# Performance work log

Measured on AMD Instinct MI355X. Metric: run time of the kernel, lower is better.

Reference implementation:

```python
import jax, jax.numpy as jnp
import numpy as np

A, U, ANT, D2, H = 128, 8, 64, 64, 256
NUE = A * U            # 1024 ues
E_INT = A * NUE        # 131072 interferes edges (all ap x ue pairs)
E_DL = NUE             # one d_link edge per ue


def _mlp(x, Wa, ba, Wb, bb):
    return jax.nn.relu(x @ Wa + ba) @ Wb + bb


def setup_inputs() -> dict:
    key = jax.random.key(0)
    ks = jax.random.split(key, 14)
    f32 = jnp.float32
    inp = {
        'pl_int_re': jax.random.normal(ks[0], (E_INT, ANT), f32) * 0.1,
        'pl_int_im': jax.random.normal(ks[1], (E_INT, ANT), f32) * 0.1,
        'pl_dl_re': jax.random.normal(ks[2], (E_DL, ANT), f32) * 0.1,
        'pl_dl_im': jax.random.normal(ks[3], (E_DL, ANT), f32) * 0.1,
        'pv_re': jax.random.normal(ks[4], (A, U, ANT), f32) * 0.1,
        'pv_im': jax.random.normal(ks[5], (A, U, ANT), f32) * 0.1,
        'W2a': jax.random.normal(ks[6], (4 * ANT, H), f32) / np.sqrt(4 * ANT),
        'b2a': jnp.zeros((H,), f32),
        'W2b': jax.random.normal(ks[7], (H, D2), f32) / np.sqrt(H),
        'b2b': jnp.zeros((D2,), f32),
        'W1a': jax.random.normal(ks[8], (1 + 2 * ANT + D2, H), f32) / np.sqrt(1 + 2 * ANT + D2),
        'b1a': jnp.zeros((H,), f32),
        'W1b': jax.random.normal(ks[9], (H, 2 * ANT), f32) / np.sqrt(H),
        'b1b': jnp.zeros((2 * ANT,), f32),
        # interferes: every ap -> every ue
        'int_src': jnp.repeat(jnp.arange(A, dtype=jnp.int32), NUE),
        'int_dst': jnp.tile(jnp.arange(NUE, dtype=jnp.int32), A),
        # d_link: ap a -> ues [a*U, (a+1)*U)
        'dl_src': jnp.repeat(jnp.arange(A, dtype=jnp.int32), U),
        'dl_dst': jnp.arange(NUE, dtype=jnp.int32),
    }
    return inp


def reference(pl_int_re, pl_int_im, pl_dl_re, pl_dl_im, pv_re, pv_im,
              W2a, b2a, W2b, b2b, W1a, b1a, W1b, b1b,
              int_src, int_dst, dl_src, dl_dst):
    pv = jax.lax.complex(pv_re, pv_im)            # [A,U,ANT] ap power_vector
    pl_int = jax.lax.complex(pl_int_re, pl_int_im)  # [E_INT,ANT]
    pl_dl = jax.lax.complex(pl_dl_re, pl_dl_im)     # [E_DL,ANT]

    def aggregate_interferes(pv_cur):
        src_sum = jnp.sum(pv_cur, axis=1)[int_src]              # [E,ANT]
        infer_vec = src_sum.conj() * pl_int                      # [E,ANT]
        sum_ap = jnp.sum(jnp.abs(infer_vec) ** 2, axis=-1)       # ||.||^2 -> [E]
        return jax.ops.segment_sum(sum_ap[:, None], int_dst, num_segments=NUE)  # [NUE,1]

    # 1) aggregate_interferes (stored in graph; recomputed at the end)
    _ = aggregate_interferes(pv)

    # 2) mlp_aggregate_interferes
    src_sum = jnp.sum(pv, axis=1)[int_src]                       # [E,ANT] complex
    feats = jnp.concatenate([pl_int, src_sum], axis=1)           # [E,2*ANT] complex
    cat_feats = jnp.concatenate([feats.real, feats.imag], axis=1)  # [E,4*ANT]
    msg2 = _mlp(cat_feats, W2a, b2a, W2b, b2b)                   # [E,D2]
    mlp_ue_all = jax.ops.segment_sum(msg2, int_dst, num_segments=NUE)  # [NUE,D2]

    # 3) update_ue_power_vector (d_link edges)
    src_pv_dl = pv[dl_src]                                       # [E_DL,U,ANT]
    iner = jnp.einsum('eua,ea->eu', src_pv_dl.conj(), pl_dl)     # bmm -> [E_DL,U]
    norm1 = jnp.abs(iner) ** 2                                   # [E_DL,U]
    mask1 = jnp.ones((E_DL, U), norm1.dtype).at[jnp.arange(E_DL), dl_dst % U].set(0.0)
    in_infer = jnp.sum(norm1 * mask1, axis=1)[:, None]           # [E_DL,1]

    feat1 = jnp.concatenate([in_infer, pl_dl.real, pl_dl.imag, mlp_ue_all[dl_dst]], axis=1)
    out1 = _mlp(feat1, W1a, b1a, W1b, b1b).reshape(E_DL, 2, ANT)  # [E_DL,2,ANT]
    ue_pv_msg = jax.lax.complex(out1[:, 0, :], out1[:, 1, :])    # [E_DL,ANT]
    # each ue receives exactly one message
    ue_pv = jnp.zeros((NUE, ANT), ue_pv_msg.dtype).at[dl_dst].set(ue_pv_msg)

    # 4) update_ap_power_vector (u_link: ue i -> ap i//U; mailbox [A,U,ANT])
    mailbox = ue_pv.reshape(A, U, ANT)
    flat = mailbox.reshape(A, U * ANT)
    row_sums = jnp.sum(jnp.abs(flat), axis=-1, keepdims=True)
    pv_new = (flat / row_sums).reshape(A, U, ANT)

    # 5) final aggregate_interferes with updated power vectors
    ue_all_interference = aggregate_interferes(pv_new)

    out_stacked = jnp.stack([pv_new.real, pv_new.imag])          # [2,A,U,ANT]
    return out_stacked, ue_all_interference
```

## Files before the change

### kernel.cpp

```cpp
#include <hip/hip_runtime.h>
#include <hip/hip_bf16.h>
#include <hip/hip_fp16.h>

#define A_NUM 128
#define U_NUM 8
#define ANT 64
#define D2 64
#define H_DIM 256
#define NUE 1024
#define E_INT 131072

typedef __attribute__((ext_vector_type(8))) short bf16x8_t;
typedef __attribute__((ext_vector_type(4))) float f32x4_t;

static __device__ inline unsigned short f2bf(float x) {
    unsigned int u = __float_as_uint(x);
    unsigned int r = (u + 0x7fffu + ((u >> 16) & 1u)) >> 16;
    return (unsigned short)r;
}
static __device__ inline unsigned int pack2(float a, float b) {
    return (unsigned int)f2bf(a) | ((unsigned int)f2bf(b) << 16);
}
static __device__ inline float bf2f(unsigned short s) {
    return __uint_as_float(((unsigned int)s) << 16);
}

__global__ void prep_kernel(const float* __restrict__ pv_re, const float* __restrict__ pv_im,
                            const float* __restrict__ W2a, const float* __restrict__ b2a,
                            const float* __restrict__ W2b,
                            const float* __restrict__ W1a, const float* __restrict__ W1b,
                            float* __restrict__ Sa, unsigned short* __restrict__ WpT,
                            unsigned short* __restrict__ W2bT,
                            float* __restrict__ W1aT, float* __restrict__ W1bT) {
    int bid = blockIdx.x, t = threadIdx.x;
    if (bid < A_NUM) {
        __shared__ float sre[ANT], sim[ANT];
        if (t < ANT) {
            float s = 0.f;
            for (int u = 0; u < U_NUM; ++u) s += pv_re[bid * 512 + u * 64 + t];
            sre[t] = s;
        } else if (t < 2 * ANT) {
            int ant = t - ANT;
            float s = 0.f;
            for (int u = 0; u < U_NUM; ++u) s += pv_im[bid * 512 + u * 64 + ant];
            sim[ant] = s;
        }
        __syncthreads();
        float a0 = 0.f, a1 = 0.f, a2 = 0.f, a3 = 0.f;
        for (int ant = 0; ant < ANT; ant += 2) {
            a0 += sre[ant] * W2a[(64 + ant) * H_DIM + t];
            a1 += sim[ant] * W2a[(192 + ant) * H_DIM + t];
            a2 += sre[ant + 1] * W2a[(64 + ant + 1) * H_DIM + t];
            a3 += sim[ant + 1] * W2a[(192 + ant + 1) * H_DIM + t];
        }
        Sa[bid * H_DIM + t] = b2a[t] + ((a0 + a2) + (a1 + a3));
    } else if (bid < 136) {
        int base = (bid - A_NUM) * 256 + t;
        for (int i = base; i < 32768 + 16384; i += 8 * 256) {
            if (i < 32768) {
                int h = i >> 7, k = i & 127;
                int row = (k < 64) ? k : (k + 64);
                WpT[i] = f2bf(W2a[row * H_DIM + h]);
            } else {
                int i2 = i - 32768;
                int d = i2 >> 8, k2 = i2 & 255;
                W2bT[i2] = f2bf(W2b[k2 * D2 + d]);
            }
        }
    } else {
        for (int i = (bid - 136) * 256 + t; i < 53248 + 32768; i += 32 * 256) {
            if (i < 53248) {
                int k = i >> 8, h = i & 255;
                W1aT[h * 208 + k] = (k < 193) ? W1a[k * 256 + h] : 0.f;
            } else {
                int i2 = i - 53248;
                int k = i2 >> 7, c = i2 & 127;
                W1bT[c * 256 + k] = W1b[k * 128 + c];
            }
        }
    }
}

__global__ __launch_bounds__(256, 4) void mlp2_kernel(
        const float* __restrict__ plre, const float* __restrict__ plim,
        const float* __restrict__ Sa, const unsigned short* __restrict__ WpT,
        const unsigned short* __restrict__ W2bT, float* __restrict__ partial,
        unsigned short* __restrict__ Pws) {
    __shared__ __attribute__((aligned(16))) unsigned short F2[2][16 * 136];
    __shared__ __attribute__((aligned(16))) unsigned short Hl[16][264];
    int bid = blockIdx.x;
    int ac = bid >> 6, jt = bid & 63;
    int j0 = jt * 16, a0 = ac * 8;
    int t = threadIdx.x, w = t >> 6, l = t & 63, lm = l & 15, lk = l >> 4;

    bf16x8_t bfr[4][4];
#pragma unroll
    for (int ht = 0; ht < 4; ++ht)
#pragma unroll
        for (int kc = 0; kc < 4; ++kc)
            bfr[ht][kc] = *reinterpret_cast<const bf16x8_t*>(
                WpT + (w * 64 + ht * 16 + lm) * 128 + kc * 32 + lk * 8);
    bf16x8_t b2h[8];
#pragma unroll
    for (int kcl = 0; kcl < 8; ++kcl)
        b2h[kcl] = *reinterpret_cast<const bf16x8_t*>(
            W2bT + (w * 16 + lm) * 256 + kcl * 32 + lk * 8);

    int er = t >> 4, seg = t & 15;
    const float* stage_base = (seg < 8) ? plre : plim;
    int stage_off = (j0 + er) * 64 + (seg & 7) * 8;
    int fw = er * 136 + seg * 8;

    f32x4_t acc2 = (f32x4_t){0.f, 0.f, 0.f, 0.f};

    float4 s0, s1;
    {
        const float* p = stage_base + (size_t)a0 * 65536 + stage_off;
        s0 = *reinterpret_cast<const float4*>(p);
        s1 = *reinterpret_cast<const float4*>(p + 4);
        *reinterpret_cast<uint4*>(&F2[0][fw]) =
            make_uint4(pack2(s0.x, s0.y), pack2(s0.z, s0.w),
                       pack2(s1.x, s1.y), pack2(s1.z, s1.w));
    }
    {
        const float* p = stage_base + (size_t)(a0 + 1) * 65536 + stage_off;
        s0 = *reinterpret_cast<const float4*>(p);
        s1 = *reinterpret_cast<const float4*>(p + 4);
    }

    int cur = 0;
    for (int ai = 0; ai < 8; ++ai) {
        int a = a0 + ai;
        __syncthreads();
        const unsigned short* Fc = F2[cur];
        if (t < 128) {
            int er3 = t >> 3, seg3 = t & 7;
            uint4 rr = *reinterpret_cast<const uint4*>(Fc + er3 * 136 + seg3 * 8);
            uint4 ri = *reinterpret_cast<const uint4*>(Fc + er3 * 136 + 64 + seg3 * 8);
            const unsigned short* pr = (const unsigned short*)&rr;
            const unsigned short* pi = (const unsigned short*)&ri;
            unsigned int pk[4];
#pragma unroll
            for (int i = 0; i < 4; ++i) {
                float re0 = bf2f(pr[2 * i]), im0 = bf2f(pi[2 * i]);
                float re1 = bf2f(pr[2 * i + 1]), im1 = bf2f(pi[2 * i + 1]);
                unsigned short h0 = __half_as_ushort(__float2half(re0 * re0 + im0 * im0));
                unsigned short h1 = __half_as_ushort(__float2half(re1 * re1 + im1 * im1));
                pk[i] = (unsigned int)h0 | ((unsigned int)h1 << 16);
            }
            *reinterpret_cast<uint4*>(&Pws[(unsigned)(a * 1024 + j0 + er3) * 64 + seg3 * 8]) =
                make_uint4(pk[0], pk[1], pk[2], pk[3]);
        }
        f32x4_t acc1[4];
#pragma unroll
        for (int ht = 0; ht < 4; ++ht) {
            float sa = Sa[a * H_DIM + w * 64 + ht * 16 + lm];
            acc1[ht] = (f32x4_t){sa, sa, sa, sa};
        }
#pragma unroll
        for (int kc = 0; kc < 4; ++kc) {
            bf16x8_t afr = *reinterpret_cast<const bf16x8_t*>(Fc + lm * 136 + kc * 32 + lk * 8);
#pragma unroll
            for (int ht = 0; ht < 4; ++ht)
                acc1[ht] = __builtin_amdgcn_mfma_f32_16x16x32_bf16(afr, bfr[ht][kc], acc1[ht], 0, 0, 0);
        }
#pragma unroll
        for (int ht = 0; ht < 4; ++ht)
#pragma unroll
            for (int r = 0; r < 4; ++r) {
                float v = acc1[ht][r];
                Hl[lk * 4 + r][ht * 16 + lm + w * 64] = f2bf(v > 0.f ? v : 0.f);
            }
        __syncthreads();
#pragma unroll
        for (int kcl = 0; kcl < 8; ++kcl) {
            bf16x8_t a2 = *reinterpret_cast<const bf16x8_t*>(&Hl[lm][kcl * 32 + lk * 8]);
            acc2 = __builtin_amdgcn_mfma_f32_16x16x32_bf16(a2, b2h[kcl], acc2, 0, 0, 0);
        }
        if (ai < 7) {
            *reinterpret_cast<uint4*>(&F2[cur ^ 1][fw]) =
                make_uint4(pack2(s0.x, s0.y), pack2(s0.z, s0.w),
                           pack2(s1.x, s1.y), pack2(s1.z, s1.w));
            if (ai < 6) {
                const float* p = stage_base + (size_t)(a0 + ai + 2) * 65536 + stage_off;
                s0 = *reinterpret_cast<const float4*>(p);
                s1 = *reinterpret_cast<const float4*>(p + 4);
            }
            cur ^= 1;
        }
    }
#pragma unroll
    for (int r = 0; r < 4; ++r)
        partial[ac * 65536 + (j0 + lk * 4 + r) * 64 + w * 16 + lm] = acc2[r];
}

__global__ __launch_bounds__(512) void dlink_norm(
        const float* __restrict__ pv_re, const float* __restrict__ pv_im,
        const float* __restrict__ pldre, const float* __restrict__ pldim,
        const float* __restrict__ partial, const float* __restrict__ b2b,
        const float* __restrict__ W1aT, const float* __restrict__ b1a,
        const float* __restrict__ W1bT, const float* __restrict__ b1b,
        float* __restrict__ Q, float* __restrict__ out) {
    int a = blockIdx.x, t = threadIdx.x, w = t >> 6, l = t & 63;
    __shared__ float pvr[512], pvi[512], pldr[512], pldi[512];
    __shared__ float nrm[8][8];
    __shared__ __attribute__((aligned(16))) float feat[8][212];
    __shared__ __attribute__((aligned(16))) float h1[8][260];
    __shared__ float red2[2][8][128];
    __shared__ __attribute__((aligned(16))) float o1[8][128];
    __shared__ float redn[8];
    __shared__ float SshInv;

    pvr[t] = pv_re[a * 512 + t];
    pvi[t] = pv_im[a * 512 + t];
    pldr[t] = pldre[a * 512 + t];
    pldi[t] = pldim[a * 512 + t];
    {
        float acc = 128.f * b2b[t & 63];
#pragma unroll
        for (int c = 0; c < 16; ++c) acc += partial[c * 65536 + a * 512 + t];
        feat[t >> 6][129 + (t & 63)] = acc;
    }
    if (t < 152) feat[t / 19][193 + t % 19] = 0.f;
    __syncthreads();
    feat[t >> 6][1 + (t & 63)] = pldr[t];
    feat[t >> 6][65 + (t & 63)] = pldi[t];
#pragma unroll
    for (int p = 0; p < 8; ++p) {
        int idx = w * 8 + p;
        int el = idx >> 3, u = idx & 7;
        float pr = pvr[u * 64 + l], pi = pvi[u * 64 + l];
        float qr = pldr[el * 64 + l], qi = pldi[el * 64 + l];
        float ir = pr * qr + pi * qi;
        float ii = pr * qi - pi * qr;
        for (int m = 1; m < 64; m <<= 1) {
            ir += __shfl_xor(ir, m, 64);
            ii += __shfl_xor(ii, m, 64);
        }
        if (l == 0) nrm[el][u] = ir * ir + ii * ii;
    }
    __syncthreads();
    if (t < 8) {
        float s = 0.f;
        for (int u = 0; u < 8; ++u)
            if (u != t) s += nrm[t][u];
        feat[t][0] = s;
    }
    __syncthreads();
    {
        int h = t >> 1, e0 = (t & 1) * 4;
        const float4* wrow = reinterpret_cast<const float4*>(W1aT + h * 208);
        const float4* f0p = reinterpret_cast<const float4*>(&feat[e0 + 0][0]);
        const float4* f1p = reinterpret_cast<const float4*>(&feat[e0 + 1][0]);
        const float4* f2p = reinterpret_cast<const float4*>(&feat[e0 + 2][0]);
        const float4* f3p = reinterpret_cast<const float4*>(&feat[e0 + 3][0]);
        float ac0 = 0.f, ac1 = 0.f, ac2 = 0.f, ac3 = 0.f;
#pragma unroll 4
        for (int kq = 0; kq < 52; ++kq) {
            float4 wv = wrow[kq];
            float4 f0 = f0p[kq], f1 = f1p[kq], f2 = f2p[kq], f3 = f3p[kq];
            ac0 = fmaf(wv.x, f0.x, ac0); ac0 = fmaf(wv.y, f0.y, ac0);
            ac0 = fmaf(wv.z, f0.z, ac0); ac0 = fmaf(wv.w, f0.w, ac0);
            ac1 = fmaf(wv.x, f1.x, ac1); ac1 = fmaf(wv.y, f1.y, ac1);
            ac1 = fmaf(wv.z, f1.z, ac1); ac1 = fmaf(wv.w, f1.w, ac1);
            ac2 = fmaf(wv.x, f2.x, ac2); ac2 = fmaf(wv.y, f2.y, ac2);
            ac2 = fmaf(wv.z, f2.z, ac2); ac2 = fmaf(wv.w, f2.w, ac2);
            ac3 = fmaf(wv.x, f3.x, ac3); ac3 = fmaf(wv.y, f3.y, ac3);
            ac3 = fmaf(wv.z, f3.z, ac3); ac3 = fmaf(wv.w, f3.w, ac3);
        }
        float bb = b1a[h];
        float s0 = bb + ac0, s1 = bb + ac1, s2 = bb + ac2, s3 = bb + ac3;
        h1[e0 + 0][h] = s0 > 0.f ? s0 : 0.f;
        h1[e0 + 1][h] = s1 > 0.f ? s1 : 0.f;
        h1[e0 + 2][h] = s2 > 0.f ? s2 : 0.f;
        h1[e0 + 3][h] = s3 > 0.f ? s3 : 0.f;
    }
    __syncthreads();
    {
        int e0 = (t & 1) * 4, c = (t >> 1) & 127, kh = t >> 8;
        const float4* wrow = reinterpret_cast<const float4*>(W1bT + c * 256 + kh * 128);
        const float4* g0 = reinterpret_cast<const float4*>(&h1[e0 + 0][kh * 128]);
        const float4* g1 = reinterpret_cast<const float4*>(&h1[e0 + 1][kh * 128]);
        const float4* g2 = reinterpret_cast<const float4*>(&h1[e0 + 2][kh * 128]);
        const float4* g3 = reinterpret_cast<const float4*>(&h1[e0 + 3][kh * 128]);
        float ac0 = 0.f, ac1 = 0.f, ac2 = 0.f, ac3 = 0.f;
#pragma unroll 4
        for (int kq = 0; kq < 32; ++kq) {
            float4 wv = wrow[kq];
            float4 f0 = g0[kq], f1 = g1[kq], f2 = g2[kq], f3 = g3[kq];
            ac0 = fmaf(wv.x, f0.x, ac0); ac0 = fmaf(wv.y, f0.y, ac0);
            ac0 = fmaf(wv.z, f0.z, ac0); ac0 = fmaf(wv.w, f0.w, ac0);
            ac1 = fmaf(wv.x, f1.x, ac1); ac1 = fmaf(wv.y, f1.y, ac1);
            ac1 = fmaf(wv.z, f1.z, ac1); ac1 = fmaf(wv.w, f1.w, ac1);
            ac2 = fmaf(wv.x, f2.x, ac2); ac2 = fmaf(wv.y, f2.y, ac2);
            ac2 = fmaf(wv.z, f2.z, ac2); ac2 = fmaf(wv.w, f2.w, ac2);
            ac3 = fmaf(wv.x, f3.x, ac3); ac3 = fmaf(wv.y, f3.y, ac3);
            ac3 = fmaf(wv.z, f3.z, ac3); ac3 = fmaf(wv.w, f3.w, ac3);
        }
        red2[kh][e0 + 0][c] = ac0;
        red2[kh][e0 + 1][c] = ac1;
        red2[kh][e0 + 2][c] = ac2;
        red2[kh][e0 + 3][c] = ac3;
    }
    __syncthreads();
    {
        int i0 = t, i1 = t + 512;
        o1[i0 >> 7][i0 & 127] = b1b[i0 & 127] + red2[0][i0 >> 7][i0 & 127] + red2[1][i0 >> 7][i0 & 127];
        o1[i1 >> 7][i1 & 127] = b1b[i1 & 127] + red2[0][i1 >> 7][i1 & 127] + red2[1][i1 >> 7][i1 & 127];
    }
    __syncthreads();
    {
        int el = t >> 6, ant = t & 63;
        float re = o1[el][ant], im = o1[el][64 + ant];
        float v = sqrtf(re * re + im * im);
        for (int m = 1; m < 64; m <<= 1) v += __shfl_xor(v, m, 64);
        if (l == 0) redn[w] = v;
    }
    __syncthreads();
    if (t == 0) {
        float S = redn[0] + redn[1] + redn[2] + redn[3] +
                  redn[4] + redn[5] + redn[6] + redn[7];
        SshInv = 1.f / S;
    }
    __syncthreads();
    {
        float inv = SshInv;
        int el = t >> 6, ant = t & 63;
        out[a * 512 + t] = o1[el][ant] * inv;
        out[65536 + a * 512 + t] = o1[el][64 + ant] * inv;
        if (t < 64) {
            float sr = 0.f, si = 0.f;
#pragma unroll
            for (int u = 0; u < 8; ++u) {
                sr += o1[u][t];
                si += o1[u][64 + t];
            }
            sr *= inv;
            si *= inv;
            Q[a * 64 + t] = sr * sr + si * si;
        }
    }
}

__global__ __launch_bounds__(256) void final_agg(const unsigned short* __restrict__ Pws,
                                                 const float* __restrict__ Qv,
                                                 float* __restrict__ out) {
    int bid = blockIdx.x, t = threadIdx.x, w = t >> 6, l = t & 63;
    __shared__ __attribute__((aligned(16))) float Qc[128][68];
    for (int i = t; i < 8192; i += 256) Qc[i >> 6][i & 63] = Qv[i];
    __syncthreads();
    int j = bid * 4 + w;
    int as = l >> 3, og = l & 7;
    float acc = 0.f;
#pragma unroll 4
    for (int ab = 0; ab < 16; ++ab) {
        int aa = ab * 8 + as;
        uint4 pv4 = *reinterpret_cast<const uint4*>(&Pws[(unsigned)(aa * 1024 + j) * 64 + og * 8]);
        float4 q0 = *reinterpret_cast<const float4*>(&Qc[aa][og * 8]);
        float4 q1 = *reinterpret_cast<const float4*>(&Qc[aa][og * 8 + 4]);
        const unsigned short* hp = (const unsigned short*)&pv4;
        acc += __half2float(__ushort_as_half(hp[0])) * q0.x;
        acc += __half2float(__ushort_as_half(hp[1])) * q0.y;
        acc += __half2float(__ushort_as_half(hp[2])) * q0.z;
        acc += __half2float(__ushort_as_half(hp[3])) * q0.w;
        acc += __half2float(__ushort_as_half(hp[4])) * q1.x;
        acc += __half2float(__ushort_as_half(hp[5])) * q1.y;
        acc += __half2float(__ushort_as_half(hp[6])) * q1.z;
        acc += __half2float(__ushort_as_half(hp[7])) * q1.w;
    }
    for (int m = 1; m < 64; m <<= 1) acc += __shfl_xor(acc, m, 64);
    if (l == 0) out[131072 + j] = acc;
}

extern "C" void kernel_launch(void* const* d_in, const int* in_sizes, int n_in,
                              void* d_out, int out_size, void* d_ws, size_t ws_size,
                              hipStream_t stream) {
    const float* plre = (const float*)d_in[0];
    const float* plim = (const float*)d_in[1];
    const float* pldre = (const float*)d_in[2];
    const float* pldim = (const float*)d_in[3];
    const float* pvre = (const float*)d_in[4];
    const float* pvim = (const float*)d_in[5];
    const float* W2a = (const float*)d_in[6];
    const float* b2a = (const float*)d_in[7];
    const float* W2b = (const float*)d_in[8];
    const float* b2b = (const float*)d_in[9];
    const float* W1a = (const float*)d_in[10];
    const float* b1a = (const float*)d_in[11];
    const float* W1b = (const float*)d_in[12];
    const float* b1b = (const float*)d_in[13];

    char* ws = (char*)d_ws;
    float* Sa = (float*)(ws);
    unsigned short* WpT = (unsigned short*)(ws + 131072);
    unsigned short* W2bT = (unsigned short*)(ws + 196608);
    float* Q = (float*)(ws + 229376);
    float* partial = (float*)(ws + 262144);
    unsigned short* Pws = (unsigned short*)(ws + 4456448);
    float* W1aT = (float*)(ws + 21233664);
    float* W1bT = (float*)(ws + 21446656);
    float* out = (float*)d_out;

    prep_kernel<<<168, 256, 0, stream>>>(pvre, pvim, W2a, b2a, W2b, W1a, W1b,
                                         Sa, WpT, W2bT, W1aT, W1bT);
    mlp2_kernel<<<1024, 256, 0, stream>>>(plre, plim, Sa, WpT, W2bT, partial, Pws);
    dlink_norm<<<128, 512, 0, stream>>>(pvre, pvim, pldre, pldim, partial, b2b,
                                        W1aT, b1a, W1bT, b1b, Q, out);
    final_agg<<<256, 256, 0, stream>>>(Pws, Q, out);
}
```

Measured before the change: 78.70 us.

## Split hidden dim across 8 waves, load A-fragments directly, reduce partials via LDS

```diff
diff --git a/kernel.cpp b/kernel.cpp
--- a/kernel.cpp
+++ b/kernel.cpp
@@ -21,8 +21,17 @@
 static __device__ inline unsigned int pack2(float a, float b) {
     return (unsigned int)f2bf(a) | ((unsigned int)f2bf(b) << 16);
 }
-static __device__ inline float bf2f(unsigned short s) {
-    return __uint_as_float(((unsigned int)s) << 16);
+static __device__ inline bf16x8_t pack8(float4 a, float4 b) {
+    union { unsigned int u[4]; bf16x8_t v; } r;
+    r.u[0] = pack2(a.x, a.y);
+    r.u[1] = pack2(a.z, a.w);
+    r.u[2] = pack2(b.x, b.y);
+    r.u[3] = pack2(b.z, b.w);
+    return r.v;
+}
+static __device__ inline unsigned int packh2(float a, float b) {
+    return (unsigned int)__half_as_ushort(__float2half(a)) |
+           ((unsigned int)__half_as_ushort(__float2half(b)) << 16);
 }
 
 __global__ void prep_kernel(const float* __restrict__ pv_re, const float* __restrict__ pv_im,
@@ -81,117 +90,110 @@
     }
 }
 
-__global__ __launch_bounds__(256, 4) void mlp2_kernel(
+__global__ __launch_bounds__(512, 4) void mlp2_kernel(
         const float* __restrict__ plre, const float* __restrict__ plim,
         const float* __restrict__ Sa, const unsigned short* __restrict__ WpT,
         const unsigned short* __restrict__ W2bT, float* __restrict__ partial,
         unsigned short* __restrict__ Pws) {
-    __shared__ __attribute__((aligned(16))) unsigned short F2[2][16 * 136];
-    __shared__ __attribute__((aligned(16))) unsigned short Hl[16][264];
+    __shared__ __attribute__((aligned(16))) float smraw[8 * 16 * 68];
     int bid = blockIdx.x;
     int ac = bid >> 6, jt = bid & 63;
     int j0 = jt * 16, a0 = ac * 8;
     int t = threadIdx.x, w = t >> 6, l = t & 63, lm = l & 15, lk = l >> 4;
-
-    bf16x8_t bfr[4][4];
-#pragma unroll
-    for (int ht = 0; ht < 4; ++ht)
+    int h0 = w * 32;
+
+    bf16x8_t bfr[2][4];
+#pragma unroll
+    for (int ht = 0; ht < 2; ++ht)
 #pragma unroll
         for (int kc = 0; kc < 4; ++kc)
             bfr[ht][kc] = *reinterpret_cast<const bf16x8_t*>(
-                WpT + (w * 64 + ht * 16 + lm) * 128 + kc * 32 + lk * 8);
-    bf16x8_t b2h[8];
-#pragma unroll
-    for (int kcl = 0; kcl < 8; ++kcl)
-        b2h[kcl] = *reinterpret_cast<const bf16x8_t*>(
-            W2bT + (w * 16 + lm) * 256 + kcl * 32 + lk * 8);
-
-    int er = t >> 4, seg = t & 15;
-    const float* stage_base = (seg < 8) ? plre : plim;
-    int stage_off = (j0 + er) * 64 + (seg & 7) * 8;
-    int fw = er * 136 + seg * 8;
-
-    f32x4_t acc2 = (f32x4_t){0.f, 0.f, 0.f, 0.f};
-
-    float4 s0, s1;
-    {
-        const float* p = stage_base + (size_t)a0 * 65536 + stage_off;
-        s0 = *reinterpret_cast<const float4*>(p);
-        s1 = *reinterpret_cast<const float4*>(p + 4);
-        *reinterpret_cast<uint4*>(&F2[0][fw]) =
-            make_uint4(pack2(s0.x, s0.y), pack2(s0.z, s0.w),
-                       pack2(s1.x, s1.y), pack2(s1.z, s1.w));
-    }
-    {
-        const float* p = stage_base + (size_t)(a0 + 1) * 65536 + stage_off;
-        s0 = *reinterpret_cast<const float4*>(p);
-        s1 = *reinterpret_cast<const float4*>(p + 4);
-    }
-
-    int cur = 0;
+                WpT + (h0 + ht * 16 + lm) * 128 + kc * 32 + lk * 8);
+    bf16x8_t b2h[4];
+#pragma unroll
+    for (int dt = 0; dt < 4; ++dt)
+        b2h[dt] = *reinterpret_cast<const bf16x8_t*>(
+            W2bT + (dt * 16 + lm) * 256 + h0 + lk * 8);
+
+    unsigned short* Hw = reinterpret_cast<unsigned short*>(smraw) + w * (16 * 40);
+    f32x4_t acc2[4];
+#pragma unroll
+    for (int dt = 0; dt < 4; ++dt) acc2[dt] = (f32x4_t){0.f, 0.f, 0.f, 0.f};
+
     for (int ai = 0; ai < 8; ++ai) {
         int a = a0 + ai;
-        __syncthreads();
-        const unsigned short* Fc = F2[cur];
-        if (t < 128) {
-            int er3 = t >> 3, seg3 = t & 7;
-            uint4 rr = *reinterpret_cast<const uint4*>(Fc + er3 * 136 + seg3 * 8);
-            uint4 ri = *reinterpret_cast<const uint4*>(Fc + er3 * 136 + 64 + seg3 * 8);
-            const unsigned short* pr = (const unsigned short*)&rr;
-            const unsigned short* pi = (const unsigned short*)&ri;
-            unsigned int pk[4];
-#pragma unroll
-            for (int i = 0; i < 4; ++i) {
-                float re0 = bf2f(pr[2 * i]), im0 = bf2f(pi[2 * i]);
-                float re1 = bf2f(pr[2 * i + 1]), im1 = bf2f(pi[2 * i + 1]);
-                unsigned short h0 = __half_as_ushort(__float2half(re0 * re0 + im0 * im0));
-                unsigned short h1 = __half_as_ushort(__float2half(re1 * re1 + im1 * im1));
-                pk[i] = (unsigned int)h0 | ((unsigned int)h1 << 16);
-            }
-            *reinterpret_cast<uint4*>(&Pws[(unsigned)(a * 1024 + j0 + er3) * 64 + seg3 * 8]) =
-                make_uint4(pk[0], pk[1], pk[2], pk[3]);
-        }
-        f32x4_t acc1[4];
-#pragma unroll
-        for (int ht = 0; ht < 4; ++ht) {
-            float sa = Sa[a * H_DIM + w * 64 + ht * 16 + lm];
-            acc1[ht] = (f32x4_t){sa, sa, sa, sa};
-        }
-#pragma unroll
-        for (int kc = 0; kc < 4; ++kc) {
-            bf16x8_t afr = *reinterpret_cast<const bf16x8_t*>(Fc + lm * 136 + kc * 32 + lk * 8);
-#pragma unroll
-            for (int ht = 0; ht < 4; ++ht)
-                acc1[ht] = __builtin_amdgcn_mfma_f32_16x16x32_bf16(afr, bfr[ht][kc], acc1[ht], 0, 0, 0);
-        }
-#pragma unroll
-        for (int ht = 0; ht < 4; ++ht)
-#pragma unroll
-            for (int r = 0; r < 4; ++r) {
-                float v = acc1[ht][r];
-                Hl[lk * 4 + r][ht * 16 + lm + w * 64] = f2bf(v > 0.f ? v : 0.f);
-            }
-        __syncthreads();
-#pragma unroll
-        for (int kcl = 0; kcl < 8; ++kcl) {
-            bf16x8_t a2 = *reinterpret_cast<const bf16x8_t*>(&Hl[lm][kcl * 32 + lk * 8]);
-            acc2 = __builtin_amdgcn_mfma_f32_16x16x32_bf16(a2, b2h[kcl], acc2, 0, 0, 0);
-        }
-        if (ai < 7) {
-            *reinterpret_cast<uint4*>(&F2[cur ^ 1][fw]) =
-                make_uint4(pack2(s0.x, s0.y), pack2(s0.z, s0.w),
-                           pack2(s1.x, s1.y), pack2(s1.z, s1.w));
-            if (ai < 6) {
-                const float* p = stage_base + (size_t)(a0 + ai + 2) * 65536 + stage_off;
-                s0 = *reinterpret_cast<const float4*>(p);
-                s1 = *reinterpret_cast<const float4*>(p + 4);
-            }
-            cur ^= 1;
-        }
-    }
-#pragma unroll
-    for (int r = 0; r < 4; ++r)
-        partial[ac * 65536 + (j0 + lk * 4 + r) * 64 + w * 16 + lm] = acc2[r];
+        const float* rowre = plre + (size_t)(a * 1024 + j0 + lm) * 64;
+        const float* rowim = plim + (size_t)(a * 1024 + j0 + lm) * 64;
+        float4 r0 = *reinterpret_cast<const float4*>(rowre + lk * 8);
+        float4 r1 = *reinterpret_cast<const float4*>(rowre + lk * 8 + 4);
+        float4 r2 = *reinterpret_cast<const float4*>(rowre + 32 + lk * 8);
+        float4 r3 = *reinterpret_cast<const float4*>(rowre + 32 + lk * 8 + 4);
+        float4 i0 = *reinterpret_cast<const float4*>(rowim + lk * 8);
+        float4 i1 = *reinterpret_cast<const float4*>(rowim + lk * 8 + 4);
+        float4 i2 = *reinterpret_cast<const float4*>(rowim + 32 + lk * 8);
+        float4 i3 = *reinterpret_cast<const float4*>(rowim + 32 + lk * 8 + 4);
+
+        if (w == 0) {
+            unsigned short* pd = Pws + (unsigned)(a * 1024 + j0 + lm) * 64 + lk * 8;
+            *reinterpret_cast<uint4*>(pd) = make_uint4(
+                packh2(r0.x * r0.x + i0.x * i0.x, r0.y * r0.y + i0.y * i0.y),
+                packh2(r0.z * r0.z + i0.z * i0.z, r0.w * r0.w + i0.w * i0.w),
+                packh2(r1.x * r1.x + i1.x * i1.x, r1.y * r1.y + i1.y * i1.y),
+                packh2(r1.z * r1.z + i1.z * i1.z, r1.w * r1.w + i1.w * i1.w));
+            *reinterpret_cast<uint4*>(pd + 32) = make_uint4(
+                packh2(r2.x * r2.x + i2.x * i2.x, r2.y * r2.y + i2.y * i2.y),
+                packh2(r2.z * r2.z + i2.z * i2.z, r2.w * r2.w + i2.w * i2.w),
+                packh2(r3.x * r3.x + i3.x * i3.x, r3.y * r3.y + i3.y * i3.y),
+                packh2(r3.z * r3.z + i3.z * i3.z, r3.w * r3.w + i3.w * i3.w));
+        }
+
+        bf16x8_t fa0 = pack8(r0, r1);
+        bf16x8_t fa1 = pack8(r2, r3);
+        bf16x8_t fa2 = pack8(i0, i1);
+        bf16x8_t fa3 = pack8(i2, i3);
+
+        float sa0 = Sa[a * H_DIM + h0 + lm];
+        float sa1 = Sa[a * H_DIM + h0 + 16 + lm];
+        f32x4_t acc1a = (f32x4_t){sa0, sa0, sa0, sa0};
+        f32x4_t acc1b = (f32x4_t){sa1, sa1, sa1, sa1};
+        acc1a = __builtin_amdgcn_mfma_f32_16x16x32_bf16(fa0, bfr[0][0], acc1a, 0, 0, 0);
+        acc1b = __builtin_amdgcn_mfma_f32_16x16x32_bf16(fa0, bfr[1][0], acc1b, 0, 0, 0);
+        acc1a = __builtin_amdgcn_mfma_f32_16x16x32_bf16(fa1, bfr[0][1], acc1a, 0, 0, 0);
+        acc1b = __builtin_amdgcn_mfma_f32_16x16x32_bf16(fa1, bfr[1][1], acc1b, 0, 0, 0);
+        acc1a = __builtin_amdgcn_mfma_f32_16x16x32_bf16(fa2, bfr[0][2], acc1a, 0, 0, 0);
+        acc1b = __builtin_amdgcn_mfma_f32_16x16x32_bf16(fa2, bfr[1][2], acc1b, 0, 0, 0);
+        acc1a = __builtin_amdgcn_mfma_f32_16x16x32_bf16(fa3, bfr[0][3], acc1a, 0, 0, 0);
+        acc1b = __builtin_amdgcn_mfma_f32_16x16x32_bf16(fa3, bfr[1][3], acc1b, 0, 0, 0);
+
+#pragma unroll
+        for (int r = 0; r < 4; ++r) {
+            int j = lk * 4 + r;
+            float va = acc1a[r], vb = acc1b[r];
+            Hw[j * 40 + lm] = f2bf(va > 0.f ? va : 0.f);
+            Hw[j * 40 + 16 + lm] = f2bf(vb > 0.f ? vb : 0.f);
+        }
+        bf16x8_t a2 = *reinterpret_cast<const bf16x8_t*>(Hw + lm * 40 + lk * 8);
+#pragma unroll
+        for (int dt = 0; dt < 4; ++dt)
+            acc2[dt] = __builtin_amdgcn_mfma_f32_16x16x32_bf16(a2, b2h[dt], acc2[dt], 0, 0, 0);
+    }
+
+    __syncthreads();
+    float* red = smraw;
+#pragma unroll
+    for (int dt = 0; dt < 4; ++dt)
+#pragma unroll
+        for (int r = 0; r < 4; ++r)
+            red[(w * 16 + lk * 4 + r) * 68 + dt * 16 + lm] = acc2[dt][r];
+    __syncthreads();
+    for (int i = t; i < 1024; i += 512) {
+        int j = i >> 6, d = i & 63;
+        float s0 = red[(0 * 16 + j) * 68 + d] + red[(1 * 16 + j) * 68 + d];
+        float s1 = red[(2 * 16 + j) * 68 + d] + red[(3 * 16 + j) * 68 + d];
+        float s2 = red[(4 * 16 + j) * 68 + d] + red[(5 * 16 + j) * 68 + d];
+        float s3 = red[(6 * 16 + j) * 68 + d] + red[(7 * 16 + j) * 68 + d];
+        partial[ac * 65536 + (j0 + j) * 64 + d] = (s0 + s1) + (s2 + s3);
+    }
 }
 
 __global__ __launch_bounds__(512) void dlink_norm(
@@ -266,7 +268,7 @@
             ac2 = fmaf(wv.x, f2.x, ac2); ac2 = fmaf(wv.y, f2.y, ac2);
             ac2 = fmaf(wv.z, f2.z, ac2); ac2 = fmaf(wv.w, f2.w, ac2);
             ac3 = fmaf(wv.x, f3.x, ac3); ac3 = fmaf(wv.y, f3.y, ac3);
-            ac3 = fmaf(wv.z, f3.z, ac3); ac3 = fmaf(wv.w, f3.w, ac3);
+            ac3 = fmaf(wv.w, f3.w, ac3); ac3 = fmaf(wv.z, f3.z, ac3);
         }
         float bb = b1a[h];
         float s0 = bb + ac0, s1 = bb + ac1, s2 = bb + ac2, s3 = bb + ac3;
@@ -403,7 +405,7 @@
 
     prep_kernel<<<168, 256, 0, stream>>>(pvre, pvim, W2a, b2a, W2b, W1a, W1b,
                                          Sa, WpT, W2bT, W1aT, W1bT);
-    mlp2_kernel<<<1024, 256, 0, stream>>>(plre, plim, Sa, WpT, W2bT, partial, Pws);
+    mlp2_kernel<<<1024, 512, 0, stream>>>(plre, plim, Sa, WpT, W2bT, partial, Pws);
     dlink_norm<<<128, 512, 0, stream>>>(pvre, pvim, pldre, pldim, partial, b2b,
                                         W1aT, b1a, W1bT, b1b, Q, out);
     final_agg<<<256, 256, 0, stream>>>(Pws, Q, out);
```

Result: slower. 111.2 us (+41.3%).

## Retile mlp2 kernel: split hidden dim across blocks, stage MFMA-fragment weights in LDS

Applied to the files above, without the earlier changes.

```diff
diff --git a/kernel.cpp b/kernel.cpp
--- a/kernel.cpp
+++ b/kernel.cpp
@@ -21,16 +21,17 @@
 static __device__ inline unsigned int pack2(float a, float b) {
     return (unsigned int)f2bf(a) | ((unsigned int)f2bf(b) << 16);
 }
-static __device__ inline float bf2f(unsigned short s) {
-    return __uint_as_float(((unsigned int)s) << 16);
+static __device__ inline unsigned int packh2(float a, float b) {
+    return (unsigned int)__half_as_ushort(__float2half(a)) |
+           ((unsigned int)__half_as_ushort(__float2half(b)) << 16);
 }
 
 __global__ void prep_kernel(const float* __restrict__ pv_re, const float* __restrict__ pv_im,
                             const float* __restrict__ W2a, const float* __restrict__ b2a,
                             const float* __restrict__ W2b,
                             const float* __restrict__ W1a, const float* __restrict__ W1b,
-                            float* __restrict__ Sa, unsigned short* __restrict__ WpT,
-                            unsigned short* __restrict__ W2bT,
+                            float* __restrict__ Sa, unsigned short* __restrict__ WpF,
+                            unsigned short* __restrict__ W2bF,
                             float* __restrict__ W1aT, float* __restrict__ W1bT) {
     int bid = blockIdx.x, t = threadIdx.x;
     if (bid < A_NUM) {
@@ -56,15 +57,21 @@
         Sa[bid * H_DIM + t] = b2a[t] + ((a0 + a2) + (a1 + a3));
     } else if (bid < 136) {
         int base = (bid - A_NUM) * 256 + t;
-        for (int i = base; i < 32768 + 16384; i += 8 * 256) {
-            if (i < 32768) {
-                int h = i >> 7, k = i & 127;
+        for (int f = base; f < 32768 + 16384; f += 8 * 256) {
+            if (f < 32768) {
+                int i = f & 7, lml = (f >> 3) & 15, lkl = (f >> 7) & 3;
+                int kc = (f >> 9) & 3, ht = (f >> 11) & 1, w = (f >> 12) & 3, hh = (f >> 14) & 1;
+                int h = hh * 128 + w * 32 + ht * 16 + lml;
+                int k = kc * 32 + lkl * 8 + i;
                 int row = (k < 64) ? k : (k + 64);
-                WpT[i] = f2bf(W2a[row * H_DIM + h]);
+                WpF[f] = f2bf(W2a[row * H_DIM + h]);
             } else {
-                int i2 = i - 32768;
-                int d = i2 >> 8, k2 = i2 & 255;
-                W2bT[i2] = f2bf(W2b[k2 * D2 + d]);
+                int f2 = f - 32768;
+                int i = f2 & 7, lml = (f2 >> 3) & 15, lkl = (f2 >> 7) & 3;
+                int dt = (f2 >> 9) & 3, w = (f2 >> 11) & 3, hh = (f2 >> 13) & 1;
+                int d = dt * 16 + lml;
+                int k = hh * 128 + w * 32 + lkl * 8 + i;
+                W2bF[f2] = f2bf(W2b[k * D2 + d]);
             }
         }
     } else {
@@ -81,117 +88,161 @@
     }
 }
 
-__global__ __launch_bounds__(256, 4) void mlp2_kernel(
+__global__ __launch_bounds__(256) void mlp2_kernel(
         const float* __restrict__ plre, const float* __restrict__ plim,
-        const float* __restrict__ Sa, const unsigned short* __restrict__ WpT,
-        const unsigned short* __restrict__ W2bT, float* __restrict__ partial,
+        const float* __restrict__ Sa, const unsigned short* __restrict__ WpF,
+        const unsigned short* __restrict__ W2bF, float* __restrict__ partial,
         unsigned short* __restrict__ Pws) {
-    __shared__ __attribute__((aligned(16))) unsigned short F2[2][16 * 136];
-    __shared__ __attribute__((aligned(16))) unsigned short Hl[16][264];
+    __shared__ __attribute__((aligned(16))) unsigned short Wl[16384];
+    __shared__ __attribute__((aligned(16))) unsigned short W2l[8192];
+    __shared__ __attribute__((aligned(16))) unsigned short F2[2][4352];
+    __shared__ __attribute__((aligned(16))) unsigned short Hw_all[4][1280];
     int bid = blockIdx.x;
-    int ac = bid >> 6, jt = bid & 63;
-    int j0 = jt * 16, a0 = ac * 8;
+    int ac = bid >> 6, hh = (bid >> 5) & 1, jt = bid & 31;
+    int j0 = jt * 32, a0 = ac * 8;
     int t = threadIdx.x, w = t >> 6, l = t & 63, lm = l & 15, lk = l >> 4;
 
-    bf16x8_t bfr[4][4];
-#pragma unroll
-    for (int ht = 0; ht < 4; ++ht)
-#pragma unroll
-        for (int kc = 0; kc < 4; ++kc)
-            bfr[ht][kc] = *reinterpret_cast<const bf16x8_t*>(
-                WpT + (w * 64 + ht * 16 + lm) * 128 + kc * 32 + lk * 8);
-    bf16x8_t b2h[8];
-#pragma unroll
-    for (int kcl = 0; kcl < 8; ++kcl)
-        b2h[kcl] = *reinterpret_cast<const bf16x8_t*>(
-            W2bT + (w * 16 + lm) * 256 + kcl * 32 + lk * 8);
-
-    int er = t >> 4, seg = t & 15;
-    const float* stage_base = (seg < 8) ? plre : plim;
-    int stage_off = (j0 + er) * 64 + (seg & 7) * 8;
-    int fw = er * 136 + seg * 8;
-
-    f32x4_t acc2 = (f32x4_t){0.f, 0.f, 0.f, 0.f};
-
-    float4 s0, s1;
-    {
-        const float* p = stage_base + (size_t)a0 * 65536 + stage_off;
+    {
+        const uint4* srcW = reinterpret_cast<const uint4*>(WpF + hh * 16384);
+        const uint4* srcW2 = reinterpret_cast<const uint4*>(W2bF + hh * 8192);
+        uint4* dW = reinterpret_cast<uint4*>(Wl);
+        uint4* dW2 = reinterpret_cast<uint4*>(W2l);
+        for (int q = t; q < 3072; q += 256) {
+            if (q < 2048) dW[q] = srcW[q];
+            else dW2[q - 2048] = srcW2[q - 2048];
+        }
+    }
+
+    int er = t >> 3, sg = t & 7;
+    const float* sb = (sg < 4) ? plre : plim;
+    int soff = (j0 + er) * 64 + (sg & 3) * 16;
+    int fw = er * 136 + sg * 16;
+
+    unsigned short* Hw = Hw_all[w];
+    f32x4_t acc2[4][2];
+#pragma unroll
+    for (int dt = 0; dt < 4; ++dt)
+#pragma unroll
+        for (int jg = 0; jg < 2; ++jg) acc2[dt][jg] = (f32x4_t){0.f, 0.f, 0.f, 0.f};
+
+    float4 s0, s1, s2, s3;
+    {
+        const float* p = sb + (size_t)a0 * 65536 + soff;
         s0 = *reinterpret_cast<const float4*>(p);
         s1 = *reinterpret_cast<const float4*>(p + 4);
+        s2 = *reinterpret_cast<const float4*>(p + 8);
+        s3 = *reinterpret_cast<const float4*>(p + 12);
         *reinterpret_cast<uint4*>(&F2[0][fw]) =
             make_uint4(pack2(s0.x, s0.y), pack2(s0.z, s0.w),
                        pack2(s1.x, s1.y), pack2(s1.z, s1.w));
-    }
-    {
-        const float* p = stage_base + (size_t)(a0 + 1) * 65536 + stage_off;
+        *reinterpret_cast<uint4*>(&F2[0][fw + 8]) =
+            make_uint4(pack2(s2.x, s2.y), pack2(s2.z, s2.w),
+                       pack2(s3.x, s3.y), pack2(s3.z, s3.w));
+    }
+    {
+        const float* p = sb + (size_t)(a0 + 1) * 65536 + soff;
         s0 = *reinterpret_cast<const float4*>(p);
         s1 = *reinterpret_cast<const float4*>(p + 4);
-    }
+        s2 = *reinterpret_cast<const float4*>(p + 8);
+        s3 = *reinterpret_cast<const float4*>(p + 12);
+    }
+    __syncthreads();
 
     int cur = 0;
     for (int ai = 0; ai < 8; ++ai) {
         int a = a0 + ai;
-        __syncthreads();
         const unsigned short* Fc = F2[cur];
-        if (t < 128) {
-            int er3 = t >> 3, seg3 = t & 7;
-            uint4 rr = *reinterpret_cast<const uint4*>(Fc + er3 * 136 + seg3 * 8);
-            uint4 ri = *reinterpret_cast<const uint4*>(Fc + er3 * 136 + 64 + seg3 * 8);
+
+        if (hh == 0) {
+            uint4 rr = *reinterpret_cast<const uint4*>(Fc + er * 136 + sg * 8);
+            uint4 ri = *reinterpret_cast<const uint4*>(Fc + er * 136 + 64 + sg * 8);
             const unsigned short* pr = (const unsigned short*)&rr;
             const unsigned short* pi = (const unsigned short*)&ri;
             unsigned int pk[4];
 #pragma unroll
             for (int i = 0; i < 4; ++i) {
-                float re0 = bf2f(pr[2 * i]), im0 = bf2f(pi[2 * i]);
-                float re1 = bf2f(pr[2 * i + 1]), im1 = bf2f(pi[2 * i + 1]);
-                unsigned short h0 = __half_as_ushort(__float2half(re0 * re0 + im0 * im0));
-                unsigned short h1 = __half_as_ushort(__float2half(re1 * re1 + im1 * im1));
-                pk[i] = (unsigned int)h0 | ((unsigned int)h1 << 16);
-            }
-            *reinterpret_cast<uint4*>(&Pws[(unsigned)(a * 1024 + j0 + er3) * 64 + seg3 * 8]) =
+                float re0 = __uint_as_float(((unsigned int)pr[2 * i]) << 16);
+                float im0 = __uint_as_float(((unsigned int)pi[2 * i]) << 16);
+                float re1 = __uint_as_float(((unsigned int)pr[2 * i + 1]) << 16);
+                float im1 = __uint_as_float(((unsigned int)pi[2 * i + 1]) << 16);
+                pk[i] = packh2(re0 * re0 + im0 * im0, re1 * re1 + im1 * im1);
+            }
+            *reinterpret_cast<uint4*>(&Pws[(unsigned)(a * 1024 + j0 + er) * 64 + sg * 8]) =
                 make_uint4(pk[0], pk[1], pk[2], pk[3]);
         }
-        f32x4_t acc1[4];
-#pragma unroll
-        for (int ht = 0; ht < 4; ++ht) {
-            float sa = Sa[a * H_DIM + w * 64 + ht * 16 + lm];
-            acc1[ht] = (f32x4_t){sa, sa, sa, sa};
-        }
+
+        float sa0 = Sa[a * H_DIM + hh * 128 + w * 32 + lm];
+        float sa1 = Sa[a * H_DIM + hh * 128 + w * 32 + 16 + lm];
+        f32x4_t acc1[2][2];
+        acc1[0][0] = (f32x4_t){sa0, sa0, sa0, sa0};
+        acc1[1][0] = acc1[0][0];
+        acc1[0][1] = (f32x4_t){sa1, sa1, sa1, sa1};
+        acc1[1][1] = acc1[0][1];
 #pragma unroll
         for (int kc = 0; kc < 4; ++kc) {
-            bf16x8_t afr = *reinterpret_cast<const bf16x8_t*>(Fc + lm * 136 + kc * 32 + lk * 8);
-#pragma unroll
-            for (int ht = 0; ht < 4; ++ht)
-                acc1[ht] = __builtin_amdgcn_mfma_f32_16x16x32_bf16(afr, bfr[ht][kc], acc1[ht], 0, 0, 0);
-        }
-#pragma unroll
-        for (int ht = 0; ht < 4; ++ht)
-#pragma unroll
-            for (int r = 0; r < 4; ++r) {
-                float v = acc1[ht][r];
-                Hl[lk * 4 + r][ht * 16 + lm + w * 64] = f2bf(v > 0.f ? v : 0.f);
-            }
-        __syncthreads();
-#pragma unroll
-        for (int kcl = 0; kcl < 8; ++kcl) {
-            bf16x8_t a2 = *reinterpret_cast<const bf16x8_t*>(&Hl[lm][kcl * 32 + lk * 8]);
-            acc2 = __builtin_amdgcn_mfma_f32_16x16x32_bf16(a2, b2h[kcl], acc2, 0, 0, 0);
+            bf16x8_t b0 = *reinterpret_cast<const bf16x8_t*>(Wl + ((w * 2 + 0) * 4 + kc) * 512 + l * 8);
+            bf16x8_t b1 = *reinterpret_cast<const bf16x8_t*>(Wl + ((w * 2 + 1) * 4 + kc) * 512 + l * 8);
+            bf16x8_t aA = *reinterpret_cast<const bf16x8_t*>(Fc + lm * 136 + kc * 32 + lk * 8);
+            bf16x8_t aB = *reinterpret_cast<const bf16x8_t*>(Fc + (16 + lm) * 136 + kc * 32 + lk * 8);
+            acc1[0][0] = __builtin_amdgcn_mfma_f32_16x16x32_bf16(aA, b0, acc1[0][0], 0, 0, 0);
+            acc1[0][1] = __builtin_amdgcn_mfma_f32_16x16x32_bf16(aA, b1, acc1[0][1], 0, 0, 0);
+            acc1[1][0] = __builtin_amdgcn_mfma_f32_16x16x32_bf16(aB, b0, acc1[1][0], 0, 0, 0);
+            acc1[1][1] = __builtin_amdgcn_mfma_f32_16x16x32_bf16(aB, b1, acc1[1][1], 0, 0, 0);
+        }
+#pragma unroll
+        for (int jg = 0; jg < 2; ++jg)
+#pragma unroll
+            for (int ht = 0; ht < 2; ++ht)
+#pragma unroll
+                for (int r = 0; r < 4; ++r) {
+                    float v = acc1[jg][ht][r];
+                    Hw[(jg * 16 + lk * 4 + r) * 40 + ht * 16 + lm] = f2bf(v > 0.f ? v : 0.f);
+                }
+        {
+            bf16x8_t a20 = *reinterpret_cast<const bf16x8_t*>(Hw + lm * 40 + lk * 8);
+            bf16x8_t a21 = *reinterpret_cast<const bf16x8_t*>(Hw + (16 + lm) * 40 + lk * 8);
+#pragma unroll
+            for (int dt = 0; dt < 4; ++dt) {
+                bf16x8_t b2 = *reinterpret_cast<const bf16x8_t*>(W2l + (w * 4 + dt) * 512 + l * 8);
+                acc2[dt][0] = __builtin_amdgcn_mfma_f32_16x16x32_bf16(a20, b2, acc2[dt][0], 0, 0, 0);
+                acc2[dt][1] = __builtin_amdgcn_mfma_f32_16x16x32_bf16(a21, b2, acc2[dt][1], 0, 0, 0);
+            }
         }
         if (ai < 7) {
             *reinterpret_cast<uint4*>(&F2[cur ^ 1][fw]) =
                 make_uint4(pack2(s0.x, s0.y), pack2(s0.z, s0.w),
                            pack2(s1.x, s1.y), pack2(s1.z, s1.w));
+            *reinterpret_cast<uint4*>(&F2[cur ^ 1][fw + 8]) =
+                make_uint4(pack2(s2.x, s2.y), pack2(s2.z, s2.w),
+                           pack2(s3.x, s3.y), pack2(s3.z, s3.w));
             if (ai < 6) {
-                const float* p = stage_base + (size_t)(a0 + ai + 2) * 65536 + stage_off;
+                const float* p = sb + (size_t)(a0 + ai + 2) * 65536 + soff;
                 s0 = *reinterpret_cast<const float4*>(p);
                 s1 = *reinterpret_cast<const float4*>(p + 4);
-            }
+                s2 = *reinterpret_cast<const float4*>(p + 8);
+                s3 = *reinterpret_cast<const float4*>(p + 12);
+            }
+            __syncthreads();
             cur ^= 1;
         }
     }
-#pragma unroll
-    for (int r = 0; r < 4; ++r)
-        partial[ac * 65536 + (j0 + lk * 4 + r) * 64 + w * 16 + lm] = acc2[r];
+
+    __syncthreads();
+    float* red = reinterpret_cast<float*>(Wl);
+#pragma unroll
+    for (int dt = 0; dt < 4; ++dt)
+#pragma unroll
+        for (int jg = 0; jg < 2; ++jg)
+#pragma unroll
+            for (int r = 0; r < 4; ++r)
+                red[(w * 32 + jg * 16 + lk * 4 + r) * 64 + dt * 16 + lm] = acc2[dt][jg][r];
+    __syncthreads();
+    for (int idx = t; idx < 2048; idx += 256) {
+        int j = idx >> 6, d = idx & 63;
+        float s = (red[(0 * 32 + j) * 64 + d] + red[(1 * 32 + j) * 64 + d]) +
+                  (red[(2 * 32 + j) * 64 + d] + red[(3 * 32 + j) * 64 + d]);
+        partial[(hh * 16 + ac) * 65536 + (j0 + j) * 64 + d] = s;
+    }
 }
 
 __global__ __launch_bounds__(512) void dlink_norm(
@@ -218,7 +269,7 @@
     {
         float acc = 128.f * b2b[t & 63];
 #pragma unroll
-        for (int c = 0; c < 16; ++c) acc += partial[c * 65536 + a * 512 + t];
+        for (int c = 0; c < 32; ++c) acc += partial[c * 65536 + a * 512 + t];
         feat[t >> 6][129 + (t & 63)] = acc;
     }
     if (t < 152) feat[t / 19][193 + t % 19] = 0.f;
@@ -392,18 +443,18 @@
 
     char* ws = (char*)d_ws;
     float* Sa = (float*)(ws);
-    unsigned short* WpT = (unsigned short*)(ws + 131072);
-    unsigned short* W2bT = (unsigned short*)(ws + 196608);
+    unsigned short* WpF = (unsigned short*)(ws + 131072);
+    unsigned short* W2bF = (unsigned short*)(ws + 196608);
     float* Q = (float*)(ws + 229376);
-    float* partial = (float*)(ws + 262144);
-    unsigned short* Pws = (unsigned short*)(ws + 4456448);
-    float* W1aT = (float*)(ws + 21233664);
-    float* W1bT = (float*)(ws + 21446656);
+    float* W1aT = (float*)(ws + 262144);
+    float* W1bT = (float*)(ws + 475136);
+    float* partial = (float*)(ws + 606208);
+    unsigned short* Pws = (unsigned short*)(ws + 8994816);
     float* out = (float*)d_out;
 
     prep_kernel<<<168, 256, 0, stream>>>(pvre, pvim, W2a, b2a, W2b, W1a, W1b,
-                                         Sa, WpT, W2bT, W1aT, W1bT);
-    mlp2_kernel<<<1024, 256, 0, stream>>>(plre, plim, Sa, WpT, W2bT, partial, Pws);
+                                         Sa, WpF, W2bF, W1aT, W1bT);
+    mlp2_kernel<<<1024, 256, 0, stream>>>(plre, plim, Sa, WpF, W2bF, partial, Pws);
     dlink_norm<<<128, 512, 0, stream>>>(pvre, pvim, pldre, pldim, partial, b2b,
                                         W1aT, b1a, W1bT, b1b, Q, out);
     final_agg<<<256, 256, 0, stream>>>(Pws, Q, out);
```

Result: faster. 76.42 us (-2.9%).
